# Kernel tuning notes

Measured on AMD Instinct MI355X. Metric: run time of the kernel, lower is better.

## Reference

```python
import jax, jax.numpy as jnp
import numpy as np

HIDDEN_SIZE = 256
INPUT_SIZE = 4
N_CLASSES = 2


def setup_inputs() -> dict:
    key = jax.random.key(0)
    ks = jax.random.split(key, 12)
    B, T, H, I = 64, 2048, HIDDEN_SIZE, INPUT_SIZE
    s = 0.1
    return {
        "y": jax.random.normal(ks[0], (B, T), dtype=jnp.float32),
        "W_ih0": s * jax.random.normal(ks[1], (4 * H, I), dtype=jnp.float32),
        "W_hh0": s * jax.random.normal(ks[2], (4 * H, H), dtype=jnp.float32),
        "b_ih0": s * jax.random.normal(ks[3], (4 * H,), dtype=jnp.float32),
        "b_hh0": s * jax.random.normal(ks[4], (4 * H,), dtype=jnp.float32),
        "W_ih1": s * jax.random.normal(ks[5], (4 * H, H), dtype=jnp.float32),
        "W_hh1": s * jax.random.normal(ks[6], (4 * H, H), dtype=jnp.float32),
        "b_ih1": s * jax.random.normal(ks[7], (4 * H,), dtype=jnp.float32),
        "b_hh1": s * jax.random.normal(ks[8], (4 * H,), dtype=jnp.float32),
        "W_fc": s * jax.random.normal(ks[9], (N_CLASSES, H), dtype=jnp.float32),
        "b_fc": s * jax.random.normal(ks[10], (N_CLASSES,), dtype=jnp.float32),
    }


def _lstm_cell(x, h, c, Wi, Wh, bi, bh):
    # gate order i, f, g, o (torch convention, matches explicit slicing)
    gates = x @ Wi.T + bi + h @ Wh.T + bh  # [B, 4H]
    i, f, g, o = jnp.split(gates, 4, axis=-1)
    c_new = jax.nn.sigmoid(f) * c + jax.nn.sigmoid(i) * jnp.tanh(g)
    h_new = jax.nn.sigmoid(o) * jnp.tanh(c_new)
    return h_new, c_new


def reference(y, W_ih0, W_hh0, b_ih0, b_hh0, W_ih1, W_hh1, b_ih1, b_hh1, W_fc, b_fc):
    B, T = y.shape
    H = HIDDEN_SIZE
    # Sliding-window input: window [y[t-3], y[t-2], y[t-1], y[t]] with -100 pad
    padded = jnp.pad(y, ((0, 0), (0, INPUT_SIZE - 1)), constant_values=-100.0)
    seq = jnp.stack([jnp.roll(padded, s, axis=1) for s in range(INPUT_SIZE - 1, -1, -1)], axis=-1)
    seq = seq[:, :T]  # [B, T, 4]

    def step(carry, x_t):
        h0, c0, h1, c1 = carry
        h0, c0 = _lstm_cell(x_t, h0, c0, W_ih0, W_hh0, b_ih0, b_hh0)
        h1, c1 = _lstm_cell(h0, h1, c1, W_ih1, W_hh1, b_ih1, b_hh1)
        return (h0, c0, h1, c1), h1

    z = jnp.zeros((B, H), dtype=y.dtype)
    _, hs = jax.lax.scan(step, (z, z, z, z), jnp.swapaxes(seq, 0, 1))  # hs: [T, B, H]
    lstm_out = jnp.swapaxes(hs, 0, 1)  # [B, T, H]
    out = lstm_out @ W_fc.T + b_fc  # [B, T, N_CLASSES]
    return out
```

## Files before the change

kernel.cpp:

```cpp
#include <hip/hip_runtime.h>


#define NWG 32
#define BB 64
#define TT 2048
#define HH 256
#define HS 8
#define RS 32

#define WS_H0    0
#define WS_H1    16384
#define WS_FLAGS 32768
#define WS_CNT   33280
#define WS_WIN   33296
#define WS_NZERO 33296

typedef float  f32x4  __attribute__((ext_vector_type(4)));
typedef __bf16 bf16x8 __attribute__((ext_vector_type(8)));
typedef unsigned long long u64;
typedef unsigned int u32;

__device__ __forceinline__ float sigf(float x)   { return 1.0f / (1.0f + __expf(-x)); }
__device__ __forceinline__ float tanh_f(float x) { return 2.0f / (1.0f + __expf(-2.0f * x)) - 1.0f; }

__device__ __forceinline__ int poll_or0_sc0(int* p) {
  int old;
  asm volatile("global_atomic_or %0, %1, %2, off sc0\n\t"
               "s_waitcnt vmcnt(0)"
               : "=&v"(old)
               : "v"(p), "v"(0)
               : "memory");
  return old;
}

__global__ void init_ws(u32* ws) {
  int i = blockIdx.x * blockDim.x + threadIdx.x;
  for (; i < WS_NZERO; i += gridDim.x * blockDim.x) ws[i] = 0u;
  if (blockIdx.x == 0 && threadIdx.x == 0) ((int*)ws)[WS_WIN] = -1;
}

__global__ __launch_bounds__(256, 1) void lstm2_persistent(
    const float* __restrict__ y,
    const float* __restrict__ Wih0, const float* __restrict__ Whh0,
    const float* __restrict__ bih0, const float* __restrict__ bhh0,
    const float* __restrict__ Wih1, const float* __restrict__ Whh1,
    const float* __restrict__ bih1, const float* __restrict__ bhh1,
    const float* __restrict__ Wfc,  const float* __restrict__ bfc,
    float* __restrict__ out,
    u32* __restrict__ ws)
{
  __bf16* h0buf = (__bf16*)(ws + WS_H0);
  __bf16* h1buf = (__bf16*)(ws + WS_H1);
  int*    flags = (int*)(ws + WS_FLAGS);
  int*    cnt   = (int*)(ws + WS_CNT);
  int*    winner= (int*)(ws + WS_WIN);

  const int tid  = threadIdx.x;

  __shared__ int s_w;
  if (tid == 0) {
    int xcc = __builtin_amdgcn_s_getreg(20 | (31 << 11)) & 0xF;
    int r = atomicAdd(&cnt[xcc], 1);
    if (r == NWG - 1) atomicCAS(winner, -1, xcc);
    int wv;
    while ((wv = __hip_atomic_load(winner, __ATOMIC_RELAXED,
                                   __HIP_MEMORY_SCOPE_AGENT)) == -1) {}
    s_w = (wv == xcc && r < NWG) ? r : -1;
  }
  __syncthreads();
  const int w = s_w;
  if (w < 0) return;

  const int wave = tid >> 6;
  const int lane = tid & 63;
  const int ml   = lane & 15;
  const int kq   = lane >> 4;

  __shared__ float lds_g0[RS][BB + 4];
  __shared__ float lds_g1[RS][BB + 4];
  __shared__ float s_wih0[RS][4];
  __shared__ float s_b0[RS];
  __shared__ float s_b1[RS];

  bf16x8 w0[2][8];
  bf16x8 w1[2][16];
  {
    #pragma unroll
    for (int n = 0; n < 2; n++) {
      const int r     = n * 16 + ml;
      const int d     = w * HS + (r & 7);
      const int rglob = (r >> 3) * 256 + d;
      #pragma unroll
      for (int s = 0; s < 8; s++) {
        const float* src = Whh0 + rglob * HH + s * 32 + kq * 8;
        bf16x8 f;
        #pragma unroll
        for (int j = 0; j < 8; j++) f[j] = (__bf16)src[j];
        w0[n][s] = f;
      }
      #pragma unroll
      for (int s = 0; s < 16; s++) {
        const int k = s * 32 + kq * 8;
        const float* src = (k < 256) ? (Wih1 + rglob * HH + k)
                                     : (Whh1 + rglob * HH + (k - 256));
        bf16x8 f;
        #pragma unroll
        for (int j = 0; j < 8; j++) f[j] = (__bf16)src[j];
        w1[n][s] = f;
      }
    }
  }

  if (tid < RS) {
    const int r     = tid;
    const int d     = w * HS + (r & 7);
    const int rglob = (r >> 3) * 256 + d;
    s_b0[r] = bih0[rglob] + bhh0[rglob];
    s_b1[r] = bih1[rglob] + bhh1[rglob];
    #pragma unroll
    for (int j = 0; j < 4; j++) s_wih0[r][j] = Wih0[rglob * 4 + j];
  }
  __syncthreads();

  float c0[2] = {0.f, 0.f};
  float c1[2] = {0.f, 0.f};

  const int b_epi = tid >> 2;
  const int dl    = (tid & 3) * 2;

  for (int p = 0; p < TT + 2; p++) {
    const int par  = p & 1;
    const int parm = par ^ 1;

    const bool doL0 = (p < TT);
    const bool doL1 = (p >= 1 && p <= TT);

    asm volatile("buffer_inv sc0" ::: "memory");

    bf16x8 a0[8], a1[8];
    {
      const int row = wave * 16 + ml;
      const __bf16* h0p = h0buf + (parm * NWG * BB + kq * BB + row) * HS;
      const __bf16* h1p = h1buf + (par  * NWG * BB + kq * BB + row) * HS;
      #pragma unroll
      for (int s = 0; s < 8; s++) a0[s] = *(const bf16x8*)(h0p + s * 4 * BB * HS);
      #pragma unroll
      for (int s = 0; s < 8; s++) a1[s] = *(const bf16x8*)(h1p + s * 4 * BB * HS);
    }

    float x[4];
    #pragma unroll
    for (int j = 0; j < 4; j++) {
      const int ti = p - 3 + j;
      x[j] = (ti >= 0 && doL0) ? y[b_epi * TT + ti] : -100.0f;
    }

    f32x4 acc00 = {0.f,0.f,0.f,0.f}, acc01 = {0.f,0.f,0.f,0.f};
    f32x4 acc10 = {0.f,0.f,0.f,0.f}, acc11 = {0.f,0.f,0.f,0.f};

    if (doL0) {
      #pragma unroll
      for (int s = 0; s < 8; s++) {
        acc00 = __builtin_amdgcn_mfma_f32_16x16x32_bf16(a0[s], w0[0][s], acc00, 0, 0, 0);
        acc01 = __builtin_amdgcn_mfma_f32_16x16x32_bf16(a0[s], w0[1][s], acc01, 0, 0, 0);
      }
    }
    if (doL1) {
      #pragma unroll
      for (int s = 0; s < 8; s++) {
        acc10 = __builtin_amdgcn_mfma_f32_16x16x32_bf16(a0[s], w1[0][s], acc10, 0, 0, 0);
        acc11 = __builtin_amdgcn_mfma_f32_16x16x32_bf16(a0[s], w1[1][s], acc11, 0, 0, 0);
      }
      #pragma unroll
      for (int s = 0; s < 8; s++) {
        acc10 = __builtin_amdgcn_mfma_f32_16x16x32_bf16(a1[s], w1[0][s + 8], acc10, 0, 0, 0);
        acc11 = __builtin_amdgcn_mfma_f32_16x16x32_bf16(a1[s], w1[1][s + 8], acc11, 0, 0, 0);
      }
    }

    {
      const int bb = wave * 16 + kq * 4;
      if (doL0) {
        #pragma unroll
        for (int j = 0; j < 4; j++) lds_g0[ml     ][bb + j] = acc00[j];
        #pragma unroll
        for (int j = 0; j < 4; j++) lds_g0[16 + ml][bb + j] = acc01[j];
      }
      if (doL1) {
        #pragma unroll
        for (int j = 0; j < 4; j++) lds_g1[ml     ][bb + j] = acc10[j];
        #pragma unroll
        for (int j = 0; j < 4; j++) lds_g1[16 + ml][bb + j] = acc11[j];
      }
    }
    __syncthreads();

    if (doL0) {
      float hn[2];
      #pragma unroll
      for (int e = 0; e < 2; e++) {
        const int d = dl + e;
        const float gi = lds_g0[d     ][b_epi] + s_b0[d     ]
          + s_wih0[d     ][0]*x[0] + s_wih0[d     ][1]*x[1] + s_wih0[d     ][2]*x[2] + s_wih0[d     ][3]*x[3];
        const float gf = lds_g0[8 + d ][b_epi] + s_b0[8 + d ]
          + s_wih0[8 + d ][0]*x[0] + s_wih0[8 + d ][1]*x[1] + s_wih0[8 + d ][2]*x[2] + s_wih0[8 + d ][3]*x[3];
        const float gg = lds_g0[16 + d][b_epi] + s_b0[16 + d]
          + s_wih0[16 + d][0]*x[0] + s_wih0[16 + d][1]*x[1] + s_wih0[16 + d][2]*x[2] + s_wih0[16 + d][3]*x[3];
        const float go = lds_g0[24 + d][b_epi] + s_b0[24 + d]
          + s_wih0[24 + d][0]*x[0] + s_wih0[24 + d][1]*x[1] + s_wih0[24 + d][2]*x[2] + s_wih0[24 + d][3]*x[3];
        const float cn = sigf(gf) * c0[e] + sigf(gi) * tanh_f(gg);
        c0[e] = cn;
        hn[e] = sigf(go) * tanh_f(cn);
      }
      union { __bf16 h[2]; u32 u; } pk;
      pk.h[0] = (__bf16)hn[0]; pk.h[1] = (__bf16)hn[1];
      *(u32*)(h0buf + (par * NWG * BB + w * BB + b_epi) * HS + dl) = pk.u;
    }

    if (doL1) {
      float hn[2];
      #pragma unroll
      for (int e = 0; e < 2; e++) {
        const int d = dl + e;
        const float gi = lds_g1[d     ][b_epi] + s_b1[d     ];
        const float gf = lds_g1[8 + d ][b_epi] + s_b1[8 + d ];
        const float gg = lds_g1[16 + d][b_epi] + s_b1[16 + d];
        const float go = lds_g1[24 + d][b_epi] + s_b1[24 + d];
        const float cn = sigf(gf) * c1[e] + sigf(gi) * tanh_f(gg);
        c1[e] = cn;
        hn[e] = sigf(go) * tanh_f(cn);
      }
      union { __bf16 h[2]; u32 u; } pk;
      pk.h[0] = (__bf16)hn[0]; pk.h[1] = (__bf16)hn[1];
      *(u32*)(h1buf + (parm * NWG * BB + w * BB + b_epi) * HS + dl) = pk.u;
    }

    asm volatile("s_waitcnt vmcnt(0)" ::: "memory");
    __syncthreads();
    if (tid == 0)
      __hip_atomic_store(&flags[w * 16], p + 2, __ATOMIC_RELAXED,
                         __HIP_MEMORY_SCOPE_WORKGROUP);

    if (p >= 2) {
      const int t = p - 2;
      const int b = 2 * w + (wave & 1);
      const int c = wave >> 1;
      const __bf16* h1r = h1buf + (par * NWG * BB + (lane >> 1) * BB + b) * HS + (lane & 1) * 4;
      union { u64 u; __bf16 h[4]; } c4; c4.u = *(const u64*)h1r;
      float s = 0.f;
      #pragma unroll
      for (int j = 0; j < 4; j++)
        s += (float)c4.h[j] * Wfc[c * HH + lane * 4 + j];
      #pragma unroll
      for (int off = 32; off > 0; off >>= 1) s += __shfl_down(s, off, 64);
      if (lane == 0) out[b * (TT * 2) + t * 2 + c] = s + bfc[c];
    }

    if (tid < NWG) {
      while (poll_or0_sc0(&flags[tid * 16]) < p + 2) {}
    }
    __syncthreads();
  }
}

extern "C" void kernel_launch(void* const* d_in, const int* in_sizes, int n_in,
                              void* d_out, int out_size, void* d_ws, size_t ws_size,
                              hipStream_t stream) {
  u32* ws = (u32*)d_ws;
  init_ws<<<dim3(64), dim3(256), 0, stream>>>(ws);
  lstm2_persistent<<<dim3(256), dim3(256), 0, stream>>>(
      (const float*)d_in[0],  (const float*)d_in[1], (const float*)d_in[2],
      (const float*)d_in[3],  (const float*)d_in[4], (const float*)d_in[5],
      (const float*)d_in[6],  (const float*)d_in[7], (const float*)d_in[8],
      (const float*)d_in[9],  (const float*)d_in[10],
      (float*)d_out, ws);
}
```

Measured before the change: 6.654 ms.

## Replace cache invalidate and atomic-or polling with sc0 loads and atomic loads

Drops the per-step buffer_inv cache invalidation. Cross-workgroup hidden-state reads now go through inline global loads with the sc0 bit, and the epilogue read becomes an agent-scope atomic load. Flag polling switches from an atomic OR to a relaxed agent-scope atomic load. The sliding input window is also kept in registers and shifted each step, so only one y value is loaded per step. The aim is to cut synchronisation and cache-maintenance cost on the serial time-step critical path, at the risk of weaker coherence guarantees if the sc0 loads can still hit stale L2/MALL data.

New measurement: 6.323 ms. 1.05x faster.

```diff
diff --git a/kernel.cpp b/kernel.cpp
--- a/kernel.cpp
+++ b/kernel.cpp
@@ -22,16 +22,6 @@
 
 __device__ __forceinline__ float sigf(float x)   { return 1.0f / (1.0f + __expf(-x)); }
 __device__ __forceinline__ float tanh_f(float x) { return 2.0f / (1.0f + __expf(-2.0f * x)) - 1.0f; }
-
-__device__ __forceinline__ int poll_or0_sc0(int* p) {
-  int old;
-  asm volatile("global_atomic_or %0, %1, %2, off sc0\n\t"
-               "s_waitcnt vmcnt(0)"
-               : "=&v"(old)
-               : "v"(p), "v"(0)
-               : "memory");
-  return old;
-}
 
 __global__ void init_ws(u32* ws) {
   int i = blockIdx.x * blockDim.x + threadIdx.x;
@@ -128,14 +118,14 @@
   const int b_epi = tid >> 2;
   const int dl    = (tid & 3) * 2;
 
+  float x[4] = {-100.0f, -100.0f, -100.0f, -100.0f};
+
   for (int p = 0; p < TT + 2; p++) {
     const int par  = p & 1;
     const int parm = par ^ 1;
 
     const bool doL0 = (p < TT);
     const bool doL1 = (p >= 1 && p <= TT);
-
-    asm volatile("buffer_inv sc0" ::: "memory");
 
     bf16x8 a0[8], a1[8];
     {
@@ -143,17 +133,20 @@
       const __bf16* h0p = h0buf + (parm * NWG * BB + kq * BB + row) * HS;
       const __bf16* h1p = h1buf + (par  * NWG * BB + kq * BB + row) * HS;
       #pragma unroll
-      for (int s = 0; s < 8; s++) a0[s] = *(const bf16x8*)(h0p + s * 4 * BB * HS);
-      #pragma unroll
-      for (int s = 0; s < 8; s++) a1[s] = *(const bf16x8*)(h1p + s * 4 * BB * HS);
-    }
-
-    float x[4];
-    #pragma unroll
-    for (int j = 0; j < 4; j++) {
-      const int ti = p - 3 + j;
-      x[j] = (ti >= 0 && doL0) ? y[b_epi * TT + ti] : -100.0f;
-    }
+      for (int s = 0; s < 8; s++)
+        asm volatile("global_load_dwordx4 %0, %1, off sc0"
+                     : "=v"(a0[s]) : "v"(h0p + s * 4 * BB * HS) : "memory");
+      #pragma unroll
+      for (int s = 0; s < 8; s++)
+        asm volatile("global_load_dwordx4 %0, %1, off sc0"
+                     : "=v"(a1[s]) : "v"(h1p + s * 4 * BB * HS) : "memory");
+    }
+
+    x[0] = x[1]; x[1] = x[2]; x[2] = x[3];
+    x[3] = (p < TT) ? y[b_epi * TT + p] : -100.0f;
+
+    asm volatile("s_waitcnt vmcnt(0)" ::: "memory");
+    __builtin_amdgcn_sched_barrier(0);
 
     f32x4 acc00 = {0.f,0.f,0.f,0.f}, acc01 = {0.f,0.f,0.f,0.f};
     f32x4 acc10 = {0.f,0.f,0.f,0.f}, acc11 = {0.f,0.f,0.f,0.f};
@@ -246,7 +239,9 @@
       const int b = 2 * w + (wave & 1);
       const int c = wave >> 1;
       const __bf16* h1r = h1buf + (par * NWG * BB + (lane >> 1) * BB + b) * HS + (lane & 1) * 4;
-      union { u64 u; __bf16 h[4]; } c4; c4.u = *(const u64*)h1r;
+      union { u64 u; __bf16 h[4]; } c4;
+      c4.u = __hip_atomic_load((u64*)h1r, __ATOMIC_RELAXED,
+                               __HIP_MEMORY_SCOPE_AGENT);
       float s = 0.f;
       #pragma unroll
       for (int j = 0; j < 4; j++)
@@ -257,7 +252,8 @@
     }
 
     if (tid < NWG) {
-      while (poll_or0_sc0(&flags[tid * 16]) < p + 2) {}
+      while (__hip_atomic_load(&flags[tid * 16], __ATOMIC_RELAXED,
+                               __HIP_MEMORY_SCOPE_AGENT) < p + 2) {}
     }
     __syncthreads();
   }
```
